# Kernel tuning notes

Measured on AMD Instinct MI355X. Metric: run time of the kernel, lower is better.

## Reference

```python
import jax, jax.numpy as jnp
import numpy as np


def setup_inputs() -> dict:
    key = jax.random.key(0)
    k1, k2, k3, k4 = jax.random.split(key, 4)
    B, S, D_IN, D_OUT = 8, 32, 4096, 11008
    x = jax.random.normal(k1, (B, S, D_IN), dtype=jnp.float32)
    # int8-range quantized weight stored as int32 (values in [-128, 127])
    quantized_weight = jax.random.randint(k2, (D_OUT, D_IN), -128, 128, dtype=jnp.int32)
    scale = jax.random.uniform(k3, (1,), dtype=jnp.float32) * 0.01 + 1e-4
    bias = jax.random.normal(k4, (D_OUT,), dtype=jnp.float32)
    return {"x": x, "quantized_weight": quantized_weight, "scale": scale, "bias": bias}


def reference(x, quantized_weight, scale, bias):
    # Dequantize full weight (per-tensor scale), then dense linear: y = x @ W^T + b
    w = quantized_weight.astype(jnp.float32) * scale[0]  # [D_OUT, D_IN]
    return jnp.einsum('bsd,od->bso', x, w) + bias
```

## Files before the change

kernel.cpp:

```cpp
#include <hip/hip_runtime.h>
#include <hip/hip_bf16.h>
#include <stdint.h>


#define MM 256
#define NN 11008
#define KK 4096
#define NT 64
#define ROWB 144
#define SLOTB (32 * ROWB)
#define NSLOT 8

typedef __bf16 bf16x8 __attribute__((ext_vector_type(8)));
typedef float  f32x4  __attribute__((ext_vector_type(4)));

__global__ void cvt_x_kernel(const float* __restrict__ x, bf16x8* __restrict__ xf) {
    int i  = blockIdx.x * 256 + threadIdx.x;
    int l  = i & 63;
    int kb = (i >> 6) & 127;
    int mb = i >> 13;
    int m  = mb * 16 + (l & 15);
    int k  = kb * 32 + (l >> 4) * 8;
    const float* p = x + (size_t)m * KK + k;
    float4 v0 = *(const float4*)p;
    float4 v1 = *(const float4*)(p + 4);
    union { __bf16 b[8]; bf16x8 v; } t;
    t.b[0] = (__bf16)v0.x; t.b[1] = (__bf16)v0.y;
    t.b[2] = (__bf16)v0.z; t.b[3] = (__bf16)v0.w;
    t.b[4] = (__bf16)v1.x; t.b[5] = (__bf16)v1.y;
    t.b[6] = (__bf16)v1.z; t.b[7] = (__bf16)v1.w;
    xf[i] = t.v;
}

__global__ __launch_bounds__(256, 3) void qlin_gemm(
    const bf16x8* __restrict__ xf, const int* __restrict__ wq,
    const float* __restrict__ scale, const float* __restrict__ bias,
    float* __restrict__ out) {

    __shared__ __align__(16) char wsm[NSLOT * SLOTB];

    const int tid  = threadIdx.x;
    const int lane = tid & 63;
    const int wid  = tid >> 6;
    const int nl   = lane & 15;
    const int qh   = lane >> 4;

    const int bid   = blockIdx.x;
    const int xcd   = bid & 7;
    const int seq   = bid >> 3;
    const int strip = xcd * 43 + (seq >> 1);
    const int mh    = seq & 1;
    const int n0    = strip * 32;

    const int wr = tid >> 3;
    const int ws = tid & 7;
    const int* wsrc = wq + (size_t)(n0 + wr) * KK + ws * 8;
    const int wdst  = wr * ROWB + ws * 16;

    const int brd0 = nl * ROWB + qh * 16;
    const int brd1 = (16 + nl) * ROWB + qh * 16;

    const bf16x8* abase = xf + ((size_t)(mh * 8 + wid * 2) * 128) * 64 + lane;

    f32x4 acc[2][2] = {};
    int4   R0[2], R1[2], R2[2], R3[2];
    bf16x8 A0[4], A1[4], A2[4], A3[4];

    auto loadW = [&](int4 (&r)[2], int t) {
        const int* p = wsrc + t * 64;
        r[0] = *(const int4*)p;
        r[1] = *(const int4*)(p + 4);
    };
    auto loadA = [&](bf16x8 (&A)[4], int t) {
#pragma unroll
        for (int fmr = 0; fmr < 2; ++fmr)
#pragma unroll
            for (int kb = 0; kb < 2; ++kb)
                A[fmr * 2 + kb] = abase[((size_t)fmr * 128 + t * 2 + kb) * 64];
    };
    auto writeW = [&](const int4 (&r)[2], int slot) {
        union { __bf16 e[8]; bf16x8 v; } c;
        c.e[0] = (__bf16)(float)r[0].x; c.e[1] = (__bf16)(float)r[0].y;
        c.e[2] = (__bf16)(float)r[0].z; c.e[3] = (__bf16)(float)r[0].w;
        c.e[4] = (__bf16)(float)r[1].x; c.e[5] = (__bf16)(float)r[1].y;
        c.e[6] = (__bf16)(float)r[1].z; c.e[7] = (__bf16)(float)r[1].w;
        *(bf16x8*)(wsm + slot * SLOTB + wdst) = c.v;
    };
    auto compute = [&](const bf16x8 (&A)[4], int slot) {
        const char* B = wsm + slot * SLOTB;
#pragma unroll
        for (int kb = 0; kb < 2; ++kb) {
            bf16x8 b0 = *(const bf16x8*)(B + brd0 + kb * 64);
            bf16x8 b1 = *(const bf16x8*)(B + brd1 + kb * 64);
#pragma unroll
            for (int fmr = 0; fmr < 2; ++fmr) {
                acc[fmr][0] = __builtin_amdgcn_mfma_f32_16x16x32_bf16(
                    A[fmr * 2 + kb], b0, acc[fmr][0], 0, 0, 0);
                acc[fmr][1] = __builtin_amdgcn_mfma_f32_16x16x32_bf16(
                    A[fmr * 2 + kb], b1, acc[fmr][1], 0, 0, 0);
            }
        }
    };

    loadW(R0, 0); loadW(R1, 1); loadW(R2, 2); loadW(R3, 3);
    loadA(A0, 0); loadA(A1, 1);
    writeW(R0, 0);
    writeW(R1, 1);
    asm volatile("s_waitcnt lgkmcnt(0)" ::: "memory");
    __builtin_amdgcn_s_barrier();

#define STEP(T, AL, WL, WS, AC)                                      \
    {                                                                \
        const int t_ = (T);                                          \
        loadA(AL, (t_ + 2 < NT) ? t_ + 2 : NT - 1);                  \
        loadW(WL, (t_ + 4 < NT) ? t_ + 4 : NT - 1);                  \
        writeW(WS, (t_ + 2) & 7);                                    \
        compute(AC, t_ & 7);                                         \
        asm volatile("s_waitcnt lgkmcnt(0)" ::: "memory");           \
        __builtin_amdgcn_s_barrier();                                \
    }

#pragma unroll 1
    for (int tq = 0; tq < NT / 4; ++tq) {
        const int t0 = tq * 4;
        STEP(t0 + 0, A2, R0, R2, A0)
        STEP(t0 + 1, A3, R1, R3, A1)
        STEP(t0 + 2, A0, R2, R0, A2)
        STEP(t0 + 3, A1, R3, R1, A3)
    }
#undef STEP

    const float sc = scale[0];
    const int erow0 = qh * 4;
#pragma unroll
    for (int fn = 0; fn < 2; ++fn) {
        const int n = n0 + fn * 16 + nl;
        const float bv = bias[n];
#pragma unroll
        for (int fmr = 0; fmr < 2; ++fmr) {
            const int m = mh * 128 + wid * 32 + fmr * 16 + erow0;
#pragma unroll
            for (int r = 0; r < 4; ++r)
                out[(size_t)(m + r) * NN + n] = acc[fmr][fn][r] * sc + bv;
        }
    }
}

extern "C" void kernel_launch(void* const* d_in, const int* in_sizes, int n_in,
                              void* d_out, int out_size, void* d_ws, size_t ws_size,
                              hipStream_t stream) {
    const float* x     = (const float*)d_in[0];
    const int*   wq    = (const int*)d_in[1];
    const float* scale = (const float*)d_in[2];
    const float* bias  = (const float*)d_in[3];
    float* out = (float*)d_out;
    bf16x8* xf = (bf16x8*)d_ws;

    cvt_x_kernel<<<dim3(MM * KK / (256 * 8)), dim3(256), 0, stream>>>(x, xf);
    qlin_gemm<<<dim3(688), dim3(256), 0, stream>>>(xf, wq, scale, bias, out);
}
```

Measured before the change: 60.33 us.

## Split K across two blocks with partial-sum workspace and reduce kernel

Adds a split-K path that doubles the grid to 1376 blocks, each covering half of K, and writes fp32 partial sums to workspace. A separate reduce kernel adds the two partials and applies scale and bias. LDS slots are cut from 8 to 4 and launch bounds raised to 4 blocks per SM to increase occupancy. The aim is more parallelism and latency hiding on the weight stream, at the cost of writing and reading about 22 MB of partials plus an extra launch. The path is used only when the workspace is large enough.

```diff
diff --git a/kernel.cpp b/kernel.cpp
--- a/kernel.cpp
+++ b/kernel.cpp
@@ -6,10 +6,9 @@
 #define MM 256
 #define NN 11008
 #define KK 4096
-#define NT 64
 #define ROWB 144
 #define SLOTB (32 * ROWB)
-#define NSLOT 8
+#define NSLOT 4
 
 typedef __bf16 bf16x8 __attribute__((ext_vector_type(8)));
 typedef float  f32x4  __attribute__((ext_vector_type(4)));
@@ -32,10 +31,10 @@
     xf[i] = t.v;
 }
 
-__global__ __launch_bounds__(256, 3) void qlin_gemm(
+__global__ __launch_bounds__(256, 4) void qlin_gemm(
     const bf16x8* __restrict__ xf, const int* __restrict__ wq,
     const float* __restrict__ scale, const float* __restrict__ bias,
-    float* __restrict__ out) {
+    float* __restrict__ out, float* __restrict__ pws, int splitk) {
 
     __shared__ __align__(16) char wsm[NSLOT * SLOTB];
 
@@ -45,22 +44,26 @@
     const int nl   = lane & 15;
     const int qh   = lane >> 4;
 
-    const int bid   = blockIdx.x;
-    const int xcd   = bid & 7;
-    const int seq   = bid >> 3;
-    const int strip = xcd * 43 + (seq >> 1);
-    const int mh    = seq & 1;
-    const int n0    = strip * 32;
+    const int bid = blockIdx.x;
+    const int xcd = bid & 7;
+    const int seq = bid >> 3;
+    int strip, mh, kh;
+    if (splitk) { strip = xcd * 43 + (seq >> 2); mh = seq & 1; kh = (seq >> 1) & 1; }
+    else        { strip = xcd * 43 + (seq >> 1); mh = seq & 1; kh = 0; }
+    const int n0 = strip * 32;
+    const int nt = splitk ? 32 : 64;
+    const int k0 = kh << 11;
+    const int aoff = kh << 6;
 
     const int wr = tid >> 3;
     const int ws = tid & 7;
-    const int* wsrc = wq + (size_t)(n0 + wr) * KK + ws * 8;
+    const int* wsrc = wq + (size_t)(n0 + wr) * KK + k0 + ws * 8;
     const int wdst  = wr * ROWB + ws * 16;
 
     const int brd0 = nl * ROWB + qh * 16;
     const int brd1 = (16 + nl) * ROWB + qh * 16;
 
-    const bf16x8* abase = xf + ((size_t)(mh * 8 + wid * 2) * 128) * 64 + lane;
+    const bf16x8* abase = xf + ((size_t)(mh * 8 + wid * 2) * 128 + aoff) * 64 + lane;
 
     f32x4 acc[2][2] = {};
     int4   R0[2], R1[2], R2[2], R3[2];
@@ -112,16 +115,16 @@
 #define STEP(T, AL, WL, WS, AC)                                      \
     {                                                                \
         const int t_ = (T);                                          \
-        loadA(AL, (t_ + 2 < NT) ? t_ + 2 : NT - 1);                  \
-        loadW(WL, (t_ + 4 < NT) ? t_ + 4 : NT - 1);                  \
-        writeW(WS, (t_ + 2) & 7);                                    \
-        compute(AC, t_ & 7);                                         \
+        loadA(AL, (t_ + 2 < nt) ? t_ + 2 : nt - 1);                  \
+        loadW(WL, (t_ + 4 < nt) ? t_ + 4 : nt - 1);                  \
+        writeW(WS, (t_ + 2) & 3);                                    \
+        compute(AC, t_ & 3);                                         \
         asm volatile("s_waitcnt lgkmcnt(0)" ::: "memory");           \
         __builtin_amdgcn_s_barrier();                                \
     }
 
 #pragma unroll 1
-    for (int tq = 0; tq < NT / 4; ++tq) {
+    for (int tq = 0; tq < (nt >> 2); ++tq) {
         const int t0 = tq * 4;
         STEP(t0 + 0, A2, R0, R2, A0)
         STEP(t0 + 1, A3, R1, R3, A1)
@@ -130,20 +133,53 @@
     }
 #undef STEP
 
+    const int erow0 = qh * 4;
+    if (splitk) {
+        float* pb = pws + (size_t)kh * (MM * NN);
+#pragma unroll
+        for (int fn = 0; fn < 2; ++fn) {
+            const int n = n0 + fn * 16 + nl;
+#pragma unroll
+            for (int fmr = 0; fmr < 2; ++fmr) {
+                const int m = mh * 128 + wid * 32 + fmr * 16 + erow0;
+#pragma unroll
+                for (int r = 0; r < 4; ++r)
+                    pb[(size_t)(m + r) * NN + n] = acc[fmr][fn][r];
+            }
+        }
+    } else {
+        const float sc = scale[0];
+#pragma unroll
+        for (int fn = 0; fn < 2; ++fn) {
+            const int n = n0 + fn * 16 + nl;
+            const float bv = bias[n];
+#pragma unroll
+            for (int fmr = 0; fmr < 2; ++fmr) {
+                const int m = mh * 128 + wid * 32 + fmr * 16 + erow0;
+#pragma unroll
+                for (int r = 0; r < 4; ++r)
+                    out[(size_t)(m + r) * NN + n] = acc[fmr][fn][r] * sc + bv;
+            }
+        }
+    }
+}
+
+__global__ void reduce_kernel(const float* __restrict__ pws,
+                              const float* __restrict__ scale,
+                              const float* __restrict__ bias,
+                              float* __restrict__ out) {
+    const int i4 = (blockIdx.x * 256 + threadIdx.x) * 4;
+    const int n  = i4 % NN;
     const float sc = scale[0];
-    const int erow0 = qh * 4;
-#pragma unroll
-    for (int fn = 0; fn < 2; ++fn) {
-        const int n = n0 + fn * 16 + nl;
-        const float bv = bias[n];
-#pragma unroll
-        for (int fmr = 0; fmr < 2; ++fmr) {
-            const int m = mh * 128 + wid * 32 + fmr * 16 + erow0;
-#pragma unroll
-            for (int r = 0; r < 4; ++r)
-                out[(size_t)(m + r) * NN + n] = acc[fmr][fn][r] * sc + bv;
-        }
-    }
+    float4 a = *(const float4*)(pws + i4);
+    float4 b = *(const float4*)(pws + (size_t)MM * NN + i4);
+    float4 c = *(const float4*)(bias + n);
+    float4 o;
+    o.x = (a.x + b.x) * sc + c.x;
+    o.y = (a.y + b.y) * sc + c.y;
+    o.z = (a.z + b.z) * sc + c.z;
+    o.w = (a.w + b.w) * sc + c.w;
+    *(float4*)(out + i4) = o;
 }
 
 extern "C" void kernel_launch(void* const* d_in, const int* in_sizes, int n_in,
@@ -155,7 +191,16 @@
     const float* bias  = (const float*)d_in[3];
     float* out = (float*)d_out;
     bf16x8* xf = (bf16x8*)d_ws;
-
-    cvt_x_kernel<<<dim3(MM * KK / (256 * 8)), dim3(256), 0, stream>>>(x, xf);
-    qlin_gemm<<<dim3(688), dim3(256), 0, stream>>>(xf, wq, scale, bias, out);
-}
+    float* pws = (float*)((char*)d_ws + (2u << 20));
+
+    const size_t need = (2u << 20) + 2ull * MM * NN * 4ull;
+    const int splitk = (ws_size >= need) ? 1 : 0;
+
+    cvt_x_kernel<<<dim3(MM * KK / (256 * 4 * 2)), dim3(256), 0, stream>>>(x, xf);
+    if (splitk) {
+        qlin_gemm<<<dim3(1376), dim3(256), 0, stream>>>(xf, wq, scale, bias, out, pws, 1);
+        reduce_kernel<<<dim3(MM * NN / 1024), dim3(256), 0, stream>>>(pws, scale, bias, out);
+    } else {
+        qlin_gemm<<<dim3(688), dim3(256), 0, stream>>>(xf, wq, scale, bias, out, pws, 0);
+    }
+}
```

After: 70.38 us. 16.7% more time.
